# Optimization experiments

Measured on AMD Instinct MI355X. Metric: run time of the kernel, lower is better.

The kernel has to match this reference:

```python
import jax, jax.numpy as jnp
import numpy as np

NPOINT, RADIUS, NSAMPLE = 1024, 0.2, 32


def setup_inputs() -> dict:
    key = jax.random.key(0)
    ks = jax.random.split(key, 8)
    B, N, C = 16, 4096, 64
    xyz = jax.random.uniform(ks[0], (B, N, 3), jnp.float32)          # points in unit cube
    features = jax.random.normal(ks[1], (B, N, C), jnp.float32)
    W1 = jax.random.normal(ks[2], (64, C + 3), jnp.float32) * 0.05   # Conv2d(67,64,1)
    b1 = jnp.zeros((64,), jnp.float32)
    W2 = jax.random.normal(ks[3], (64, 64), jnp.float32) * 0.05      # Conv2d(64,64,1)
    b2 = jnp.zeros((64,), jnp.float32)
    W3 = jax.random.normal(ks[4], (128, 64), jnp.float32) * 0.05     # Conv2d(64,128,1)
    b3 = jnp.zeros((128,), jnp.float32)
    return {"xyz": xyz, "features": features, "W1": W1, "b1": b1,
            "W2": W2, "b2": b2, "W3": W3, "b3": b3}


def farthest_point_sampling(xyz, npoint):
    # Sequential iterative selection (classic FPS) via lax.scan.
    B, N, _ = xyz.shape
    def step(carry, _):
        dist, far = carry                                            # [B,N], [B]
        centroid = jnp.take_along_axis(xyz, far[:, None, None], axis=1)  # [B,1,3]
        d = jnp.sum((xyz - centroid) ** 2, axis=-1)                  # [B,N]
        dist = jnp.minimum(dist, d)
        nxt = jnp.argmax(dist, axis=-1).astype(jnp.int32)
        return (dist, nxt), far
    init = (jnp.full((B, N), 1e10, xyz.dtype), jnp.zeros((B,), jnp.int32))
    _, idx = jax.lax.scan(step, init, None, length=npoint)
    return idx.T                                                     # [B, npoint]


def ball_query(xyz, new_xyz, radius, nsample):
    B, N, _ = xyz.shape
    S = new_xyz.shape[1]
    sqd = jnp.sum((new_xyz[:, :, None, :] - xyz[:, None, :, :]) ** 2, axis=-1)  # [B,S,N]
    idx = jnp.broadcast_to(jnp.arange(N, dtype=jnp.int32), (B, S, N))
    idx = jnp.where(sqd > radius * radius, N, idx)
    idx = jnp.sort(idx, axis=-1)[:, :, :nsample]                     # first nsample in-ball
    first = idx[:, :, :1]
    return jnp.where(idx == N, first, idx)                           # pad with first hit


def _gather(points, idx):
    # points [B,N,C], idx [B,S,K] -> [B,S,K,C]
    B = points.shape[0]
    return points[jnp.arange(B)[:, None, None], idx]


def reference(xyz, features, W1, b1, W2, b2, W3, b3):
    fps_idx = farthest_point_sampling(xyz, NPOINT)                   # [B,S]
    new_xyz = jnp.take_along_axis(xyz, fps_idx[..., None], axis=1)   # [B,S,3]
    idx = ball_query(xyz, new_xyz, RADIUS, NSAMPLE)                  # [B,S,K]
    grouped_xyz = _gather(xyz, idx) - new_xyz[:, :, None, :]         # [B,S,K,3]
    grouped = jnp.concatenate([grouped_xyz, _gather(features, idx)], axis=-1)  # [B,S,K,3+C]
    x = jnp.transpose(grouped, (0, 3, 2, 1))                          # [B, 3+C, K, S]
    # 1x1 Conv2d stack (no activations in the original Sequential)
    x = jnp.einsum('oc,bckn->bokn', W1, x) + b1[None, :, None, None]
    x = jnp.einsum('oc,bckn->bokn', W2, x) + b2[None, :, None, None]
    x = jnp.einsum('oc,bckn->bokn', W3, x) + b3[None, :, None, None]
    new_features = jnp.max(x, axis=2)                                 # max over nsample -> [B,128,S]
    return new_xyz, new_features, fps_idx
```

## Files before the change

kernel.cpp:

```cpp
#include <hip/hip_runtime.h>
#include <cstdint>
#include <cstddef>

#define B_      16
#define N_      4096
#define CFEAT_  64
#define NPOINT_ 1024
#define NSAMPLE_ 32
#define CIN_    67
#define KPAD_   96
#define COUT_   128
#define R2_     0.04f

typedef float f32x2 __attribute__((ext_vector_type(2)));
typedef float f32x4 __attribute__((ext_vector_type(4)));
typedef short bf16x8 __attribute__((ext_vector_type(8)));

__device__ __forceinline__ f32x2 pk_sub(f32x2 a, f32x2 b) {
  f32x2 d;
  asm("v_pk_add_f32 %0, %1, %2 neg_lo:[0,1] neg_hi:[0,1]" : "=v"(d) : "v"(a), "v"(b));
  return d;
}
__device__ __forceinline__ f32x2 pk_mul(f32x2 a, f32x2 b) {
  f32x2 d;
  asm("v_pk_mul_f32 %0, %1, %2" : "=v"(d) : "v"(a), "v"(b));
  return d;
}
__device__ __forceinline__ f32x2 pk_add(f32x2 a, f32x2 b) {
  f32x2 d;
  asm("v_pk_add_f32 %0, %1, %2" : "=v"(d) : "v"(a), "v"(b));
  return d;
}
__device__ __forceinline__ float max3f(float a, float b, float c) {
  float r;
  asm("v_max3_f32 %0, %1, %2, %3" : "=v"(r) : "v"(a), "v"(b), "v"(c));
  return r;
}
__device__ __forceinline__ unsigned short f2bf(float f) {
  uint32_t u = __float_as_uint(f);
  uint32_t r = (u + 0x7FFFu + ((u >> 16) & 1u)) >> 16;
  return (unsigned short)r;
}

template<int CTRL>
__device__ __forceinline__ float dpp_fmax(float v) {
  int s = __builtin_amdgcn_update_dpp(__float_as_int(v), __float_as_int(v),
                                      CTRL, 0xF, 0xF, false);
  return fmaxf(v, __int_as_float(s));
}

__global__ __launch_bounds__(256) void k_prep(
    const float* __restrict__ xyz, float* __restrict__ xyzT) {
  int gp = blockIdx.x * 256 + threadIdx.x;
  int b = gp >> 12, p = gp & (N_ - 1);
  float x = xyz[(size_t)gp * 3 + 0];
  float y = xyz[(size_t)gp * 3 + 1];
  float z = xyz[(size_t)gp * 3 + 2];
  float* T = xyzT + (size_t)b * 3 * N_;
  T[p] = x; T[N_ + p] = y; T[2 * N_ + p] = z;
}

__global__ __launch_bounds__(256) void k_fuse(
    const float* __restrict__ W1, const float* __restrict__ b1,
    const float* __restrict__ W2, const float* __restrict__ b2,
    const float* __restrict__ W3, const float* __restrict__ b3,
    unsigned short* __restrict__ Wbf ,
    float* __restrict__ beff ) {
  __shared__ float W21[64][CIN_];
  __shared__ float b21[64];
  int t = threadIdx.x;
  for (int i = t; i < 64 * CIN_; i += 256) {
    int o = i / CIN_, c = i - o * CIN_;
    float s = 0.f;
    for (int j = 0; j < 64; ++j) s = fmaf(W2[o * 64 + j], W1[j * CIN_ + c], s);
    W21[o][c] = s;
  }
  if (t < 64) {
    float s = b2[t];
    for (int j = 0; j < 64; ++j) s = fmaf(W2[t * 64 + j], b1[j], s);
    b21[t] = s;
  }
  __syncthreads();
  for (int i = t; i < COUT_ * (KPAD_ / 2); i += 256) {
    int o = i / (KPAD_ / 2), cp = i - o * (KPAD_ / 2);
    int c0 = 2 * cp, c1 = c0 + 1;
    int s0i = (c0 < 64) ? c0 + 3 : ((c0 < 67) ? c0 - 64 : -1);
    int s1i = (c1 < 64) ? c1 + 3 : ((c1 < 67) ? c1 - 64 : -1);
    float s0 = 0.f, s1 = 0.f;
    if (s0i >= 0) {
      float a = 0.f;
      for (int j = 0; j < 64; ++j) a = fmaf(W3[o * 64 + j], W21[j][s0i], a);
      s0 = a;
    }
    if (s1i >= 0) {
      float a = 0.f;
      for (int j = 0; j < 64; ++j) a = fmaf(W3[o * 64 + j], W21[j][s1i], a);
      s1 = a;
    }
    uint32_t pk = (uint32_t)f2bf(s0) | ((uint32_t)f2bf(s1) << 16);
    ((uint32_t*)Wbf)[o * (KPAD_ / 2) + cp] = pk;
  }
  if (t < COUT_) {
    float s = b3[t];
    for (int j = 0; j < 64; ++j) s = fmaf(W3[t * 64 + j], b21[j], s);
    beff[t] = s;
  }
}

__global__ __launch_bounds__(256) void k_fps(
    const float* __restrict__ xyz,
    float* __restrict__ out_newxyz, float* __restrict__ out_fpsf) {
  int b = blockIdx.x, t = threadIdx.x;
  const float* X = xyz + (size_t)b * (N_ * 3);
  __shared__ __align__(16) float Xsh[N_ * 3];
  __shared__ __align__(16) float4 res[NPOINT_];
  __shared__ __align__(16) float4 redA[2][4];
  __shared__ __align__(16) int    redI[2][4];
  for (int i = t; i < (N_ * 3) / 4; i += 256)
    ((float4*)Xsh)[i] = ((const float4*)X)[i];
  __syncthreads();

  const int base = t * 16;
  f32x2 px[8], py[8], pz[8], dist[8];
#pragma unroll
  for (int k = 0; k < 8; ++k) {
    int j = base + 2 * k;
    px[k] = f32x2{Xsh[j * 3 + 0], Xsh[j * 3 + 3]};
    py[k] = f32x2{Xsh[j * 3 + 1], Xsh[j * 3 + 4]};
    pz[k] = f32x2{Xsh[j * 3 + 2], Xsh[j * 3 + 5]};
    dist[k] = f32x2{1e10f, 1e10f};
  }
  float cx = Xsh[0], cy = Xsh[1], cz = Xsh[2];
  if (t == 0) res[0] = make_float4(cx, cy, cz, 0.f);
  const int w = t >> 6, lane = t & 63;

  for (int it = 1; it < NPOINT_; ++it) {
    f32x2 cxx = {cx, cx}, cyy = {cy, cy}, czz = {cz, cz};
    {
#pragma clang fp contract(off)
#pragma unroll
      for (int k = 0; k < 8; ++k) {
        f32x2 dx = pk_sub(px[k], cxx);
        f32x2 dy = pk_sub(py[k], cyy);
        f32x2 dz = pk_sub(pz[k], czz);
        f32x2 s = pk_add(pk_add(pk_mul(dx, dx), pk_mul(dy, dy)), pk_mul(dz, dz));
        dist[k].x = fminf(dist[k].x, s.x);
        dist[k].y = fminf(dist[k].y, s.y);
      }
    }
    float m0 = max3f(dist[0].x, dist[0].y, dist[1].x);
    float m1 = max3f(dist[1].y, dist[2].x, dist[2].y);
    float m2 = max3f(dist[3].x, dist[3].y, dist[4].x);
    float m3 = max3f(dist[4].y, dist[5].x, dist[5].y);
    float m4 = max3f(dist[6].x, dist[6].y, dist[7].x);
    float n0 = max3f(m0, m1, m2);
    float n1 = max3f(m3, m4, dist[7].y);
    float bv = fmaxf(n0, n1);

    int jm = 15;
#pragma unroll
    for (int j = 14; j >= 0; --j) {
      float dj = (j & 1) ? dist[j >> 1].y : dist[j >> 1].x;
      jm = (dj == bv) ? j : jm;
    }
    int bi = base + jm;

    float v = bv;
    v = dpp_fmax<0xB1>(v);
    v = dpp_fmax<0x4E>(v);
    v = dpp_fmax<0x141>(v);
    v = dpp_fmax<0x140>(v);
    v = dpp_fmax<0x142>(v);
    v = dpp_fmax<0x143>(v);
    float wmax = __int_as_float(__builtin_amdgcn_readlane(__float_as_int(v), 63));
    unsigned long long msk = __ballot(bv == wmax);
    int winlane = __ffsll((long long)msk) - 1;
    int wbi = __builtin_amdgcn_readlane(bi, winlane);

    int par = it & 1;
    if (lane == 0) {
      float x = Xsh[wbi * 3 + 0], y = Xsh[wbi * 3 + 1], z = Xsh[wbi * 3 + 2];
      redA[par][w] = make_float4(wmax, x, y, z);
      redI[par][w] = wbi;
    }
    __syncthreads();
    float4 a0 = redA[par][0], a1 = redA[par][1];
    float4 a2 = redA[par][2], a3 = redA[par][3];
    int4 ii = *(const int4*)&redI[par][0];
    bool g01 = a1.x > a0.x, g23 = a3.x > a2.x;
    float4 s01 = g01 ? a1 : a0; int i01 = g01 ? ii.y : ii.x;
    float4 s23 = g23 ? a3 : a2; int i23 = g23 ? ii.w : ii.z;
    bool g = s23.x > s01.x;
    float4 s = g ? s23 : s01; int wi = g ? i23 : i01;
    cx = s.y; cy = s.z; cz = s.w;
    if (t == 0) res[it] = make_float4(cx, cy, cz, (float)wi);
  }
  __syncthreads();
  float* nx = out_newxyz + (size_t)b * (NPOINT_ * 3);
  float* nf = out_fpsf + (size_t)b * NPOINT_;
  for (int i = t; i < NPOINT_; i += 256) {
    float4 r = res[i];
    nx[i * 3 + 0] = r.x; nx[i * 3 + 1] = r.y; nx[i * 3 + 2] = r.z;
    nf[i] = r.w;
  }
}

__global__ __launch_bounds__(256) void k_group(
    const float* __restrict__ xyzT, const float* __restrict__ feat,
    const float* __restrict__ newxyz,
    const unsigned short* __restrict__ Wbf, const float* __restrict__ beff,
    float* __restrict__ outF) {
  __shared__ __align__(16) unsigned short Wl[COUT_ * KPAD_];
  __shared__ __align__(16) unsigned short gl[128 * KPAD_];
  __shared__ int   idxs[128];
  __shared__ float ctr[4][3];
  __shared__ float bsh[COUT_];
  __shared__ __align__(16) float outsh[4][COUT_];
  int t = threadIdx.x;
  int b = blockIdx.y;
  int sbase = blockIdx.x * 4;
  int w = t >> 6, lane = t & 63;

  for (int i = t; i < (COUT_ * KPAD_ * 2) / 16; i += 256)
    ((float4*)Wl)[i] = ((const float4*)Wbf)[i];
  for (int i = t; i < (128 * KPAD_ * 2) / 16; i += 256)
    ((float4*)gl)[i] = make_float4(0.f, 0.f, 0.f, 0.f);
  if (t < COUT_) bsh[t] = beff[t];

  const float* Xx = xyzT + (size_t)b * 3 * N_;
  const float* Xy = Xx + N_;
  const float* Xz = Xx + 2 * N_;

  {
#pragma clang fp contract(off)
    int s = b * NPOINT_ + sbase + w;
    float cx = newxyz[(size_t)s * 3 + 0];
    float cy = newxyz[(size_t)s * 3 + 1];
    float cz = newxyz[(size_t)s * 3 + 2];
    if (lane == 0) { ctr[w][0] = cx; ctr[w][1] = cy; ctr[w][2] = cz; }
    int total = 0, first = 0;
    float xx = Xx[lane], yy = Xy[lane], zz = Xz[lane];
    int j = 0;
    while (true) {
      int jn = j + 1;
      float nx2 = 0.f, ny2 = 0.f, nz2 = 0.f;
      if (jn < N_ / 64) {
        int pn = jn * 64 + lane;
        nx2 = Xx[pn]; ny2 = Xy[pn]; nz2 = Xz[pn];
      }
      float dx = xx - cx, dy = yy - cy, dz = zz - cz;
      float t0 = dx * dx, t1 = dy * dy, t2 = dz * dz;
      float d = (t0 + t1) + t2;
      bool inb = !(d > R2_);
      unsigned long long mask = __ballot(inb);
      if (total == 0 && mask) first = j * 64 + (__ffsll((long long)mask) - 1);
      if (inb) {
        int slot = total + __popcll(mask & ((1ull << lane) - 1ull));
        if (slot < NSAMPLE_) idxs[w * NSAMPLE_ + slot] = j * 64 + lane;
      }
      total += (int)__popcll(mask);
      if (total >= NSAMPLE_ || jn >= N_ / 64) break;
      xx = nx2; yy = ny2; zz = nz2; j = jn;
    }
    for (int slot = total + lane; slot < NSAMPLE_; slot += 64)
      idxs[w * NSAMPLE_ + slot] = first;
  }
  __syncthreads();

  for (int i = t; i < 128 * 16; i += 256) {
    int n = i >> 4, cg = i & 15;
    int p = idxs[n];
    float4 f = *(const float4*)(feat + (((size_t)b * N_ + p) * CFEAT_) + 4 * cg);
    uint32_t lo = (uint32_t)f2bf(f.x) | ((uint32_t)f2bf(f.y) << 16);
    uint32_t hi = (uint32_t)f2bf(f.z) | ((uint32_t)f2bf(f.w) << 16);
    *(uint2*)((char*)gl + n * (KPAD_ * 2) + cg * 8) = make_uint2(lo, hi);
  }
  if (t < 128) {
    int n = t, p = idxs[n];
    float x = Xx[p] - ctr[n >> 5][0];
    float y = Xy[p] - ctr[n >> 5][1];
    float z = Xz[p] - ctr[n >> 5][2];
    uint32_t lo = (uint32_t)f2bf(x) | ((uint32_t)f2bf(y) << 16);
    uint32_t hi = (uint32_t)f2bf(z);
    *(uint2*)((char*)gl + n * (KPAD_ * 2) + 128) = make_uint2(lo, hi);
  }
  __syncthreads();

  int q = lane >> 4, c16 = lane & 15;
  f32x4 acc[2][8];
#pragma unroll
  for (int tm = 0; tm < 2; ++tm)
#pragma unroll
    for (int tn = 0; tn < 8; ++tn)
#pragma unroll
      for (int j = 0; j < 4; ++j) acc[tm][tn][j] = 0.f;

  const char* Wb = (const char*)Wl;
  const char* Gb = (const char*)gl;
#pragma unroll
  for (int ks = 0; ks < 3; ++ks) {
    int cb = q * 16 + ks * 64;
    bf16x8 a0 = *(const bf16x8*)(Wb + (32 * w + c16) * (KPAD_ * 2) + cb);
    bf16x8 a1 = *(const bf16x8*)(Wb + (32 * w + 16 + c16) * (KPAD_ * 2) + cb);
#pragma unroll
    for (int tn = 0; tn < 8; ++tn) {
      bf16x8 bb = *(const bf16x8*)(Gb + (16 * tn + c16) * (KPAD_ * 2) + cb);
      acc[0][tn] = __builtin_amdgcn_mfma_f32_16x16x32_bf16(a0, bb, acc[0][tn], 0, 0, 0);
      acc[1][tn] = __builtin_amdgcn_mfma_f32_16x16x32_bf16(a1, bb, acc[1][tn], 0, 0, 0);
    }
  }

#pragma unroll
  for (int tm = 0; tm < 2; ++tm) {
#pragma unroll
    for (int si = 0; si < 4; ++si) {
      f32x4 mx;
#pragma unroll
      for (int j = 0; j < 4; ++j)
        mx[j] = fmaxf(acc[tm][2 * si][j], acc[tm][2 * si + 1][j]);
#pragma unroll
      for (int off = 1; off <= 8; off <<= 1) {
#pragma unroll
        for (int j = 0; j < 4; ++j) mx[j] = fmaxf(mx[j], __shfl_xor(mx[j], off));
      }
      if (c16 == 0)
        *(f32x4*)&outsh[si][32 * w + 16 * tm + 4 * q] = mx;
    }
  }
  __syncthreads();
  if (t < COUT_) {
    float bb2 = bsh[t];
    float4 v = make_float4(outsh[0][t] + bb2, outsh[1][t] + bb2,
                           outsh[2][t] + bb2, outsh[3][t] + bb2);
    *(float4*)&outF[((size_t)b * COUT_ + t) * NPOINT_ + sbase] = v;
  }
}

extern "C" void kernel_launch(void* const* d_in, const int* in_sizes, int n_in,
                              void* d_out, int out_size, void* d_ws, size_t ws_size,
                              hipStream_t stream) {
  (void)in_sizes; (void)n_in; (void)out_size; (void)ws_size;
  const float* xyz  = (const float*)d_in[0];
  const float* feat = (const float*)d_in[1];
  const float* W1 = (const float*)d_in[2];
  const float* b1 = (const float*)d_in[3];
  const float* W2 = (const float*)d_in[4];
  const float* b2 = (const float*)d_in[5];
  const float* W3 = (const float*)d_in[6];
  const float* b3 = (const float*)d_in[7];

  float* out = (float*)d_out;
  float* out_newxyz = out;
  float* out_feat   = out + (size_t)B_ * NPOINT_ * 3;
  float* out_fpsf   = out_feat + (size_t)B_ * COUT_ * NPOINT_;

  char* ws = (char*)d_ws;
  unsigned short* Wbf = (unsigned short*)ws;
  float* beff = (float*)(ws + (size_t)COUT_ * KPAD_ * 2);
  float* xyzT = beff + COUT_;

  k_prep<<<(B_ * N_) / 256, 256, 0, stream>>>(xyz, xyzT);
  k_fuse<<<1, 256, 0, stream>>>(W1, b1, W2, b2, W3, b3, Wbf, beff);
  k_fps<<<B_, 256, 0, stream>>>(xyz, out_newxyz, out_fpsf);
  k_group<<<dim3(NPOINT_ / 4, B_), 256, 0, stream>>>(xyzT, feat, out_newxyz, Wbf, beff, out_feat);
}
```

Baseline: 854.1 us.

## Fuse FPS and grouping into persistent kernel with progress-flag streaming

Measured after the change: 834.4 us. 1.02x faster.

```diff
diff --git a/kernel.cpp b/kernel.cpp
--- a/kernel.cpp
+++ b/kernel.cpp
@@ -11,6 +11,8 @@
 #define KPAD_   96
 #define COUT_   128
 #define R2_     0.04f
+#define NTASK_  (B_ * (NPOINT_ / 4))
+#define SCOPE_  __HIP_MEMORY_SCOPE_AGENT
 
 typedef float f32x2 __attribute__((ext_vector_type(2)));
 typedef float f32x4 __attribute__((ext_vector_type(4)));
@@ -41,7 +43,6 @@
   uint32_t r = (u + 0x7FFFu + ((u >> 16) & 1u)) >> 16;
   return (unsigned short)r;
 }
-
 template<int CTRL>
 __device__ __forceinline__ float dpp_fmax(float v) {
   int s = __builtin_amdgcn_update_dpp(__float_as_int(v), __float_as_int(v),
@@ -49,23 +50,11 @@
   return fmaxf(v, __int_as_float(s));
 }
 
-__global__ __launch_bounds__(256) void k_prep(
-    const float* __restrict__ xyz, float* __restrict__ xyzT) {
-  int gp = blockIdx.x * 256 + threadIdx.x;
-  int b = gp >> 12, p = gp & (N_ - 1);
-  float x = xyz[(size_t)gp * 3 + 0];
-  float y = xyz[(size_t)gp * 3 + 1];
-  float z = xyz[(size_t)gp * 3 + 2];
-  float* T = xyzT + (size_t)b * 3 * N_;
-  T[p] = x; T[N_ + p] = y; T[2 * N_ + p] = z;
-}
-
 __global__ __launch_bounds__(256) void k_fuse(
     const float* __restrict__ W1, const float* __restrict__ b1,
     const float* __restrict__ W2, const float* __restrict__ b2,
     const float* __restrict__ W3, const float* __restrict__ b3,
-    unsigned short* __restrict__ Wbf ,
-    float* __restrict__ beff ) {
+    unsigned short* __restrict__ Wbf, float* __restrict__ beff) {
   __shared__ float W21[64][CIN_];
   __shared__ float b21[64];
   int t = threadIdx.x;
@@ -107,232 +96,260 @@
   }
 }
 
-__global__ __launch_bounds__(256) void k_fps(
-    const float* __restrict__ xyz,
-    float* __restrict__ out_newxyz, float* __restrict__ out_fpsf) {
-  int b = blockIdx.x, t = threadIdx.x;
-  const float* X = xyz + (size_t)b * (N_ * 3);
-  __shared__ __align__(16) float Xsh[N_ * 3];
-  __shared__ __align__(16) float4 res[NPOINT_];
-  __shared__ __align__(16) float4 redA[2][4];
-  __shared__ __align__(16) int    redI[2][4];
-  for (int i = t; i < (N_ * 3) / 4; i += 256)
-    ((float4*)Xsh)[i] = ((const float4*)X)[i];
-  __syncthreads();
-
-  const int base = t * 16;
-  f32x2 px[8], py[8], pz[8], dist[8];
-#pragma unroll
-  for (int k = 0; k < 8; ++k) {
-    int j = base + 2 * k;
-    px[k] = f32x2{Xsh[j * 3 + 0], Xsh[j * 3 + 3]};
-    py[k] = f32x2{Xsh[j * 3 + 1], Xsh[j * 3 + 4]};
-    pz[k] = f32x2{Xsh[j * 3 + 2], Xsh[j * 3 + 5]};
-    dist[k] = f32x2{1e10f, 1e10f};
-  }
-  float cx = Xsh[0], cy = Xsh[1], cz = Xsh[2];
-  if (t == 0) res[0] = make_float4(cx, cy, cz, 0.f);
+__global__ __launch_bounds__(256) void k_mega(
+    const float* __restrict__ xyz, const float* __restrict__ feat,
+    int* __restrict__ ctrl, int* __restrict__ progress,
+    const unsigned short* __restrict__ Wbf, const float* __restrict__ beff,
+    float* __restrict__ out_newxyz, float* __restrict__ out_fpsf,
+    float* __restrict__ outF) {
+  __shared__ __align__(16) char smem[65712];
+  __shared__ int tsk_sh;
+  const int bid = blockIdx.x, t = threadIdx.x;
   const int w = t >> 6, lane = t & 63;
 
-  for (int it = 1; it < NPOINT_; ++it) {
-    f32x2 cxx = {cx, cx}, cyy = {cy, cy}, czz = {cz, cz};
+  if (bid < B_) {
+    const int b = bid;
+    float* Xsh  = (float*)smem;
+    float4* res = (float4*)(smem + 49152);
+    float4* redA = (float4*)(smem + 65536);
+    int*    redI = (int*)(smem + 65664);
+    uint32_t* nxu = (uint32_t*)(out_newxyz + (size_t)b * NPOINT_ * 3);
+    const float* X = xyz + (size_t)b * (N_ * 3);
+    for (int i = t; i < (N_ * 3) / 4; i += 256)
+      ((float4*)Xsh)[i] = ((const float4*)X)[i];
+    __syncthreads();
+
+    const int base = t * 16;
+    f32x2 px[8], py[8], pz[8], dist[8];
+#pragma unroll
+    for (int k = 0; k < 8; ++k) {
+      int j = base + 2 * k;
+      px[k] = f32x2{Xsh[j * 3 + 0], Xsh[j * 3 + 3]};
+      py[k] = f32x2{Xsh[j * 3 + 1], Xsh[j * 3 + 4]};
+      pz[k] = f32x2{Xsh[j * 3 + 2], Xsh[j * 3 + 5]};
+      dist[k] = f32x2{1e10f, 1e10f};
+    }
+    float cx = Xsh[0], cy = Xsh[1], cz = Xsh[2];
+    if (t == 0) res[0] = make_float4(cx, cy, cz, 0.f);
+
+    for (int it = 1; it < NPOINT_; ++it) {
+      if (t == 0) {
+        if ((it & 15) == 1 && it > 1)
+          __hip_atomic_store(&progress[b * 16], it - 1, __ATOMIC_RELEASE, SCOPE_);
+        int c = it - 1;
+        __hip_atomic_store(&nxu[c * 3 + 0], __float_as_uint(cx), __ATOMIC_RELAXED, SCOPE_);
+        __hip_atomic_store(&nxu[c * 3 + 1], __float_as_uint(cy), __ATOMIC_RELAXED, SCOPE_);
+        __hip_atomic_store(&nxu[c * 3 + 2], __float_as_uint(cz), __ATOMIC_RELAXED, SCOPE_);
+      }
+      f32x2 cxx = {cx, cx}, cyy = {cy, cy}, czz = {cz, cz};
+      {
+#pragma clang fp contract(off)
+#pragma unroll
+        for (int k = 0; k < 8; ++k) {
+          f32x2 dx = pk_sub(px[k], cxx);
+          f32x2 dy = pk_sub(py[k], cyy);
+          f32x2 dz = pk_sub(pz[k], czz);
+          f32x2 s = pk_add(pk_add(pk_mul(dx, dx), pk_mul(dy, dy)), pk_mul(dz, dz));
+          dist[k].x = fminf(dist[k].x, s.x);
+          dist[k].y = fminf(dist[k].y, s.y);
+        }
+      }
+      float m0 = max3f(dist[0].x, dist[0].y, dist[1].x);
+      float m1 = max3f(dist[1].y, dist[2].x, dist[2].y);
+      float m2 = max3f(dist[3].x, dist[3].y, dist[4].x);
+      float m3 = max3f(dist[4].y, dist[5].x, dist[5].y);
+      float m4 = max3f(dist[6].x, dist[6].y, dist[7].x);
+      float n0 = max3f(m0, m1, m2);
+      float n1 = max3f(m3, m4, dist[7].y);
+      float bv = fmaxf(n0, n1);
+
+      int jm = 15;
+#pragma unroll
+      for (int j = 14; j >= 0; --j) {
+        float dj = (j & 1) ? dist[j >> 1].y : dist[j >> 1].x;
+        jm = (dj == bv) ? j : jm;
+      }
+      int bi = base + jm;
+
+      float v = bv;
+      v = dpp_fmax<0xB1>(v);
+      v = dpp_fmax<0x4E>(v);
+      v = dpp_fmax<0x141>(v);
+      v = dpp_fmax<0x140>(v);
+      v = dpp_fmax<0x142>(v);
+      v = dpp_fmax<0x143>(v);
+      float wmax = __int_as_float(__builtin_amdgcn_readlane(__float_as_int(v), 63));
+      unsigned long long msk = __ballot(bv == wmax);
+      int winlane = __ffsll((long long)msk) - 1;
+      int wbi = __builtin_amdgcn_readlane(bi, winlane);
+
+      int par = it & 1;
+      if (lane == 0) {
+        float x = Xsh[wbi * 3 + 0], y = Xsh[wbi * 3 + 1], z = Xsh[wbi * 3 + 2];
+        redA[par * 4 + w] = make_float4(wmax, x, y, z);
+        redI[par * 4 + w] = wbi;
+      }
+      __syncthreads();
+      float4 a0 = redA[par * 4 + 0], a1 = redA[par * 4 + 1];
+      float4 a2 = redA[par * 4 + 2], a3 = redA[par * 4 + 3];
+      int4 ii = *(const int4*)&redI[par * 4];
+      bool g01 = a1.x > a0.x, g23 = a3.x > a2.x;
+      float4 s01 = g01 ? a1 : a0; int i01 = g01 ? ii.y : ii.x;
+      float4 s23 = g23 ? a3 : a2; int i23 = g23 ? ii.w : ii.z;
+      bool g = s23.x > s01.x;
+      float4 s = g ? s23 : s01; int wi = g ? i23 : i01;
+      cx = s.y; cy = s.z; cz = s.w;
+      if (t == 0) res[it] = make_float4(cx, cy, cz, (float)wi);
+    }
+    if (t == 0) {
+      __hip_atomic_store(&nxu[1023 * 3 + 0], __float_as_uint(cx), __ATOMIC_RELAXED, SCOPE_);
+      __hip_atomic_store(&nxu[1023 * 3 + 1], __float_as_uint(cy), __ATOMIC_RELAXED, SCOPE_);
+      __hip_atomic_store(&nxu[1023 * 3 + 2], __float_as_uint(cz), __ATOMIC_RELAXED, SCOPE_);
+      __hip_atomic_store(&progress[b * 16], NPOINT_, __ATOMIC_RELEASE, SCOPE_);
+    }
+    __syncthreads();
+    float* nf = out_fpsf + (size_t)b * NPOINT_;
+    for (int i = t; i < NPOINT_; i += 256) nf[i] = res[i].w;
+  }
+
+  unsigned short* Wl = (unsigned short*)smem;
+  unsigned short* gl = (unsigned short*)(smem + 24576);
+  int*   idxs = (int*)(smem + 49152);
+  float* ctrv = (float*)(smem + 49664);
+  float* bsh  = (float*)(smem + 49712);
+  float (*outsh)[COUT_] = (float(*)[COUT_])(smem + 50224);
+  for (;;) {
+    __syncthreads();
+    if (t == 0) tsk_sh = atomicAdd(&ctrl[0], 1);
+    __syncthreads();
+    int task = tsk_sh;
+    if (task >= NTASK_) break;
+    if (task < 256) {
+    }
+    int tile = task >> 4;
+    int bb = task & 15;
+    int sbase = tile * 4;
+    if (t == 0) {
+      int need = 4 * tile + 4, spins = 0;
+      while (__hip_atomic_load(&progress[bb * 16], __ATOMIC_ACQUIRE, SCOPE_) < need) {
+        __builtin_amdgcn_s_sleep(2);
+        if (++spins > (1 << 24)) break;
+      }
+    }
+    if (task == tsk_sh) {
+      for (int i = t; i < (COUT_ * KPAD_ * 2) / 16; i += 256)
+        ((float4*)Wl)[i] = ((const float4*)Wbf)[i];
+      if (t < COUT_) bsh[t] = beff[t];
+    }
+    __syncthreads();
+    for (int i = t; i < 128 * 7; i += 256) {
+      int n = i / 7, k = i - n * 7;
+      *(uint2*)((char*)gl + n * (KPAD_ * 2) + 136 + k * 8) = make_uint2(0u, 0u);
+    }
     {
 #pragma clang fp contract(off)
-#pragma unroll
-      for (int k = 0; k < 8; ++k) {
-        f32x2 dx = pk_sub(px[k], cxx);
-        f32x2 dy = pk_sub(py[k], cyy);
-        f32x2 dz = pk_sub(pz[k], czz);
-        f32x2 s = pk_add(pk_add(pk_mul(dx, dx), pk_mul(dy, dy)), pk_mul(dz, dz));
-        dist[k].x = fminf(dist[k].x, s.x);
-        dist[k].y = fminf(dist[k].y, s.y);
-      }
-    }
-    float m0 = max3f(dist[0].x, dist[0].y, dist[1].x);
-    float m1 = max3f(dist[1].y, dist[2].x, dist[2].y);
-    float m2 = max3f(dist[3].x, dist[3].y, dist[4].x);
-    float m3 = max3f(dist[4].y, dist[5].x, dist[5].y);
-    float m4 = max3f(dist[6].x, dist[6].y, dist[7].x);
-    float n0 = max3f(m0, m1, m2);
-    float n1 = max3f(m3, m4, dist[7].y);
-    float bv = fmaxf(n0, n1);
-
-    int jm = 15;
-#pragma unroll
-    for (int j = 14; j >= 0; --j) {
-      float dj = (j & 1) ? dist[j >> 1].y : dist[j >> 1].x;
-      jm = (dj == bv) ? j : jm;
-    }
-    int bi = base + jm;
-
-    float v = bv;
-    v = dpp_fmax<0xB1>(v);
-    v = dpp_fmax<0x4E>(v);
-    v = dpp_fmax<0x141>(v);
-    v = dpp_fmax<0x140>(v);
-    v = dpp_fmax<0x142>(v);
-    v = dpp_fmax<0x143>(v);
-    float wmax = __int_as_float(__builtin_amdgcn_readlane(__float_as_int(v), 63));
-    unsigned long long msk = __ballot(bv == wmax);
-    int winlane = __ffsll((long long)msk) - 1;
-    int wbi = __builtin_amdgcn_readlane(bi, winlane);
-
-    int par = it & 1;
-    if (lane == 0) {
-      float x = Xsh[wbi * 3 + 0], y = Xsh[wbi * 3 + 1], z = Xsh[wbi * 3 + 2];
-      redA[par][w] = make_float4(wmax, x, y, z);
-      redI[par][w] = wbi;
-    }
-    __syncthreads();
-    float4 a0 = redA[par][0], a1 = redA[par][1];
-    float4 a2 = redA[par][2], a3 = redA[par][3];
-    int4 ii = *(const int4*)&redI[par][0];
-    bool g01 = a1.x > a0.x, g23 = a3.x > a2.x;
-    float4 s01 = g01 ? a1 : a0; int i01 = g01 ? ii.y : ii.x;
-    float4 s23 = g23 ? a3 : a2; int i23 = g23 ? ii.w : ii.z;
-    bool g = s23.x > s01.x;
-    float4 s = g ? s23 : s01; int wi = g ? i23 : i01;
-    cx = s.y; cy = s.z; cz = s.w;
-    if (t == 0) res[it] = make_float4(cx, cy, cz, (float)wi);
-  }
-  __syncthreads();
-  float* nx = out_newxyz + (size_t)b * (NPOINT_ * 3);
-  float* nf = out_fpsf + (size_t)b * NPOINT_;
-  for (int i = t; i < NPOINT_; i += 256) {
-    float4 r = res[i];
-    nx[i * 3 + 0] = r.x; nx[i * 3 + 1] = r.y; nx[i * 3 + 2] = r.z;
-    nf[i] = r.w;
-  }
-}
-
-__global__ __launch_bounds__(256) void k_group(
-    const float* __restrict__ xyzT, const float* __restrict__ feat,
-    const float* __restrict__ newxyz,
-    const unsigned short* __restrict__ Wbf, const float* __restrict__ beff,
-    float* __restrict__ outF) {
-  __shared__ __align__(16) unsigned short Wl[COUT_ * KPAD_];
-  __shared__ __align__(16) unsigned short gl[128 * KPAD_];
-  __shared__ int   idxs[128];
-  __shared__ float ctr[4][3];
-  __shared__ float bsh[COUT_];
-  __shared__ __align__(16) float outsh[4][COUT_];
-  int t = threadIdx.x;
-  int b = blockIdx.y;
-  int sbase = blockIdx.x * 4;
-  int w = t >> 6, lane = t & 63;
-
-  for (int i = t; i < (COUT_ * KPAD_ * 2) / 16; i += 256)
-    ((float4*)Wl)[i] = ((const float4*)Wbf)[i];
-  for (int i = t; i < (128 * KPAD_ * 2) / 16; i += 256)
-    ((float4*)gl)[i] = make_float4(0.f, 0.f, 0.f, 0.f);
-  if (t < COUT_) bsh[t] = beff[t];
-
-  const float* Xx = xyzT + (size_t)b * 3 * N_;
-  const float* Xy = Xx + N_;
-  const float* Xz = Xx + 2 * N_;
-
-  {
-#pragma clang fp contract(off)
-    int s = b * NPOINT_ + sbase + w;
-    float cx = newxyz[(size_t)s * 3 + 0];
-    float cy = newxyz[(size_t)s * 3 + 1];
-    float cz = newxyz[(size_t)s * 3 + 2];
-    if (lane == 0) { ctr[w][0] = cx; ctr[w][1] = cy; ctr[w][2] = cz; }
-    int total = 0, first = 0;
-    float xx = Xx[lane], yy = Xy[lane], zz = Xz[lane];
-    int j = 0;
-    while (true) {
-      int jn = j + 1;
-      float nx2 = 0.f, ny2 = 0.f, nz2 = 0.f;
-      if (jn < N_ / 64) {
-        int pn = jn * 64 + lane;
-        nx2 = Xx[pn]; ny2 = Xy[pn]; nz2 = Xz[pn];
-      }
-      float dx = xx - cx, dy = yy - cy, dz = zz - cz;
-      float t0 = dx * dx, t1 = dy * dy, t2 = dz * dz;
-      float d = (t0 + t1) + t2;
-      bool inb = !(d > R2_);
-      unsigned long long mask = __ballot(inb);
-      if (total == 0 && mask) first = j * 64 + (__ffsll((long long)mask) - 1);
-      if (inb) {
-        int slot = total + __popcll(mask & ((1ull << lane) - 1ull));
-        if (slot < NSAMPLE_) idxs[w * NSAMPLE_ + slot] = j * 64 + lane;
-      }
-      total += (int)__popcll(mask);
-      if (total >= NSAMPLE_ || jn >= N_ / 64) break;
-      xx = nx2; yy = ny2; zz = nz2; j = jn;
-    }
-    for (int slot = total + lane; slot < NSAMPLE_; slot += 64)
-      idxs[w * NSAMPLE_ + slot] = first;
-  }
-  __syncthreads();
-
-  for (int i = t; i < 128 * 16; i += 256) {
-    int n = i >> 4, cg = i & 15;
-    int p = idxs[n];
-    float4 f = *(const float4*)(feat + (((size_t)b * N_ + p) * CFEAT_) + 4 * cg);
-    uint32_t lo = (uint32_t)f2bf(f.x) | ((uint32_t)f2bf(f.y) << 16);
-    uint32_t hi = (uint32_t)f2bf(f.z) | ((uint32_t)f2bf(f.w) << 16);
-    *(uint2*)((char*)gl + n * (KPAD_ * 2) + cg * 8) = make_uint2(lo, hi);
-  }
-  if (t < 128) {
-    int n = t, p = idxs[n];
-    float x = Xx[p] - ctr[n >> 5][0];
-    float y = Xy[p] - ctr[n >> 5][1];
-    float z = Xz[p] - ctr[n >> 5][2];
-    uint32_t lo = (uint32_t)f2bf(x) | ((uint32_t)f2bf(y) << 16);
-    uint32_t hi = (uint32_t)f2bf(z);
-    *(uint2*)((char*)gl + n * (KPAD_ * 2) + 128) = make_uint2(lo, hi);
-  }
-  __syncthreads();
-
-  int q = lane >> 4, c16 = lane & 15;
-  f32x4 acc[2][8];
-#pragma unroll
-  for (int tm = 0; tm < 2; ++tm)
-#pragma unroll
-    for (int tn = 0; tn < 8; ++tn)
-#pragma unroll
-      for (int j = 0; j < 4; ++j) acc[tm][tn][j] = 0.f;
-
-  const char* Wb = (const char*)Wl;
-  const char* Gb = (const char*)gl;
-#pragma unroll
-  for (int ks = 0; ks < 3; ++ks) {
-    int cb = q * 16 + ks * 64;
-    bf16x8 a0 = *(const bf16x8*)(Wb + (32 * w + c16) * (KPAD_ * 2) + cb);
-    bf16x8 a1 = *(const bf16x8*)(Wb + (32 * w + 16 + c16) * (KPAD_ * 2) + cb);
-#pragma unroll
-    for (int tn = 0; tn < 8; ++tn) {
-      bf16x8 bb = *(const bf16x8*)(Gb + (16 * tn + c16) * (KPAD_ * 2) + cb);
-      acc[0][tn] = __builtin_amdgcn_mfma_f32_16x16x32_bf16(a0, bb, acc[0][tn], 0, 0, 0);
-      acc[1][tn] = __builtin_amdgcn_mfma_f32_16x16x32_bf16(a1, bb, acc[1][tn], 0, 0, 0);
-    }
-  }
-
-#pragma unroll
-  for (int tm = 0; tm < 2; ++tm) {
-#pragma unroll
-    for (int si = 0; si < 4; ++si) {
-      f32x4 mx;
-#pragma unroll
-      for (int j = 0; j < 4; ++j)
-        mx[j] = fmaxf(acc[tm][2 * si][j], acc[tm][2 * si + 1][j]);
-#pragma unroll
-      for (int off = 1; off <= 8; off <<= 1) {
-#pragma unroll
-        for (int j = 0; j < 4; ++j) mx[j] = fmaxf(mx[j], __shfl_xor(mx[j], off));
-      }
-      if (c16 == 0)
-        *(f32x4*)&outsh[si][32 * w + 16 * tm + 4 * q] = mx;
-    }
-  }
-  __syncthreads();
-  if (t < COUT_) {
-    float bb2 = bsh[t];
-    float4 v = make_float4(outsh[0][t] + bb2, outsh[1][t] + bb2,
-                           outsh[2][t] + bb2, outsh[3][t] + bb2);
-    *(float4*)&outF[((size_t)b * COUT_ + t) * NPOINT_ + sbase] = v;
+      const float* X = xyz + (size_t)bb * (N_ * 3);
+      int s = bb * NPOINT_ + sbase + w;
+      uint32_t* cp = (uint32_t*)(out_newxyz) + (size_t)s * 3;
+      float cx = __uint_as_float(__hip_atomic_load(&cp[0], __ATOMIC_RELAXED, SCOPE_));
+      float cy = __uint_as_float(__hip_atomic_load(&cp[1], __ATOMIC_RELAXED, SCOPE_));
+      float cz = __uint_as_float(__hip_atomic_load(&cp[2], __ATOMIC_RELAXED, SCOPE_));
+      if (lane == 0) { ctrv[w * 3 + 0] = cx; ctrv[w * 3 + 1] = cy; ctrv[w * 3 + 2] = cz; }
+      int total = 0, first = 0;
+      float xx = X[lane * 3 + 0], yy = X[lane * 3 + 1], zz = X[lane * 3 + 2];
+      int j = 0;
+      while (true) {
+        int jn = j + 1;
+        float nx2 = 0.f, ny2 = 0.f, nz2 = 0.f;
+        if (jn < N_ / 64) {
+          int pn = jn * 64 + lane;
+          nx2 = X[pn * 3 + 0]; ny2 = X[pn * 3 + 1]; nz2 = X[pn * 3 + 2];
+        }
+        float dx = xx - cx, dy = yy - cy, dz = zz - cz;
+        float t0v = dx * dx, t1v = dy * dy, t2v = dz * dz;
+        float d = (t0v + t1v) + t2v;
+        bool inb = !(d > R2_);
+        unsigned long long mask = __ballot(inb);
+        if (total == 0 && mask) first = j * 64 + (__ffsll((long long)mask) - 1);
+        if (inb) {
+          int slot = total + __popcll(mask & ((1ull << lane) - 1ull));
+          if (slot < NSAMPLE_) idxs[w * NSAMPLE_ + slot] = j * 64 + lane;
+        }
+        total += (int)__popcll(mask);
+        if (total >= NSAMPLE_ || jn >= N_ / 64) break;
+        xx = nx2; yy = ny2; zz = nz2; j = jn;
+      }
+      for (int slot = total + lane; slot < NSAMPLE_; slot += 64)
+        idxs[w * NSAMPLE_ + slot] = first;
+    }
+    __syncthreads();
+
+    for (int i = t; i < 128 * 16; i += 256) {
+      int n = i >> 4, cg = i & 15;
+      int p = idxs[n];
+      float4 f = *(const float4*)(feat + (((size_t)bb * N_ + p) * CFEAT_) + 4 * cg);
+      uint32_t lo = (uint32_t)f2bf(f.x) | ((uint32_t)f2bf(f.y) << 16);
+      uint32_t hi = (uint32_t)f2bf(f.z) | ((uint32_t)f2bf(f.w) << 16);
+      *(uint2*)((char*)gl + n * (KPAD_ * 2) + cg * 8) = make_uint2(lo, hi);
+    }
+    if (t < 128) {
+      int n = t, p = idxs[n];
+      const float* Xp = xyz + ((size_t)bb * N_ + p) * 3;
+      float x = Xp[0] - ctrv[(n >> 5) * 3 + 0];
+      float y = Xp[1] - ctrv[(n >> 5) * 3 + 1];
+      float z = Xp[2] - ctrv[(n >> 5) * 3 + 2];
+      uint32_t lo = (uint32_t)f2bf(x) | ((uint32_t)f2bf(y) << 16);
+      uint32_t hi = (uint32_t)f2bf(z);
+      *(uint2*)((char*)gl + n * (KPAD_ * 2) + 128) = make_uint2(lo, hi);
+    }
+    __syncthreads();
+
+    int q = lane >> 4, c16 = lane & 15;
+    f32x4 acc[2][8];
+#pragma unroll
+    for (int tm = 0; tm < 2; ++tm)
+#pragma unroll
+      for (int tn = 0; tn < 8; ++tn)
+#pragma unroll
+        for (int j = 0; j < 4; ++j) acc[tm][tn][j] = 0.f;
+    const char* Wb = (const char*)Wl;
+    const char* Gb = (const char*)gl;
+#pragma unroll
+    for (int ks = 0; ks < 3; ++ks) {
+      int cb = q * 16 + ks * 64;
+      bf16x8 a0 = *(const bf16x8*)(Wb + (32 * w + c16) * (KPAD_ * 2) + cb);
+      bf16x8 a1 = *(const bf16x8*)(Wb + (32 * w + 16 + c16) * (KPAD_ * 2) + cb);
+#pragma unroll
+      for (int tn = 0; tn < 8; ++tn) {
+        bf16x8 bbv = *(const bf16x8*)(Gb + (16 * tn + c16) * (KPAD_ * 2) + cb);
+        acc[0][tn] = __builtin_amdgcn_mfma_f32_16x16x32_bf16(a0, bbv, acc[0][tn], 0, 0, 0);
+        acc[1][tn] = __builtin_amdgcn_mfma_f32_16x16x32_bf16(a1, bbv, acc[1][tn], 0, 0, 0);
+      }
+    }
+#pragma unroll
+    for (int tm = 0; tm < 2; ++tm) {
+#pragma unroll
+      for (int si = 0; si < 4; ++si) {
+        f32x4 mx;
+#pragma unroll
+        for (int j = 0; j < 4; ++j)
+          mx[j] = fmaxf(acc[tm][2 * si][j], acc[tm][2 * si + 1][j]);
+#pragma unroll
+        for (int off = 1; off <= 8; off <<= 1) {
+#pragma unroll
+          for (int j = 0; j < 4; ++j) mx[j] = fmaxf(mx[j], __shfl_xor(mx[j], off));
+        }
+        if (c16 == 0)
+          *(f32x4*)&outsh[si][32 * w + 16 * tm + 4 * q] = mx;
+      }
+    }
+    __syncthreads();
+    if (t < COUT_) {
+      float bb2 = bsh[t];
+      float4 vv = make_float4(outsh[0][t] + bb2, outsh[1][t] + bb2,
+                              outsh[2][t] + bb2, outsh[3][t] + bb2);
+      *(float4*)&outF[((size_t)bb * COUT_ + t) * NPOINT_ + sbase] = vv;
+    }
   }
 }
 
@@ -355,12 +372,13 @@
   float* out_fpsf   = out_feat + (size_t)B_ * COUT_ * NPOINT_;
 
   char* ws = (char*)d_ws;
-  unsigned short* Wbf = (unsigned short*)ws;
-  float* beff = (float*)(ws + (size_t)COUT_ * KPAD_ * 2);
-  float* xyzT = beff + COUT_;
-
-  k_prep<<<(B_ * N_) / 256, 256, 0, stream>>>(xyz, xyzT);
+  int* ctrl = (int*)ws;
+  int* progress = (int*)(ws + 256);
+  unsigned short* Wbf = (unsigned short*)(ws + 1536);
+  float* beff = (float*)(ws + 1536 + 24576);
+
+  hipMemsetAsync(ws, 0, 1536, stream);
   k_fuse<<<1, 256, 0, stream>>>(W1, b1, W2, b2, W3, b3, Wbf, beff);
-  k_fps<<<B_, 256, 0, stream>>>(xyz, out_newxyz, out_fpsf);
-  k_group<<<dim3(NPOINT_ / 4, B_), 256, 0, stream>>>(xyzT, feat, out_newxyz, Wbf, beff, out_feat);
-}
+  k_mega<<<256, 256, 0, stream>>>(xyz, feat, ctrl, progress, Wbf, beff,
+                                  out_newxyz, out_fpsf, out_feat);
+}
```
